# Kernel optimization log

Hardware: AMD Instinct MI355X
Metric: run time of the kernel (lower is better)

Reference implementation:

```python
import jax, jax.numpy as jnp
import numpy as np

D_MODEL = 768
NUM_HEADS = 12
D_K = D_MODEL // NUM_HEADS


def setup_inputs() -> dict:
    key = jax.random.key(0)
    ks = jax.random.split(key, 11)
    B, S = 2, 2048
    sc = 1.0 / np.sqrt(D_MODEL)
    return {
        "q": jax.random.normal(ks[0], (B, S, D_MODEL), jnp.float32),
        "k": jax.random.normal(ks[1], (B, S, D_MODEL), jnp.float32),
        "v": jax.random.normal(ks[2], (B, S, D_MODEL), jnp.float32),
        "w_q": jax.random.normal(ks[3], (D_MODEL, D_MODEL), jnp.float32) * sc,
        "b_q": jnp.zeros((D_MODEL,), jnp.float32),
        "w_k": jax.random.normal(ks[4], (D_MODEL, D_MODEL), jnp.float32) * sc,
        "b_k": jnp.zeros((D_MODEL,), jnp.float32),
        "w_v": jax.random.normal(ks[5], (D_MODEL, D_MODEL), jnp.float32) * sc,
        "b_v": jnp.zeros((D_MODEL,), jnp.float32),
        "w_o": jax.random.normal(ks[6], (D_MODEL, D_MODEL), jnp.float32) * sc,
        "b_o": jnp.zeros((D_MODEL,), jnp.float32),
    }


def _split_heads(x, B):
    # [B, S, D] -> [B, H, S, d_k]
    return x.reshape(B, -1, NUM_HEADS, D_K).transpose(0, 2, 1, 3)


def reference(q, k, v, w_q, b_q, w_k, b_k, w_v, b_v, w_o, b_o):
    B = q.shape[0]
    # torch nn.Linear: y = x @ W.T + b; weights stored [out, in]
    qh = _split_heads(q @ w_q.T + b_q, B)
    kh = _split_heads(k @ w_k.T + b_k, B)
    vh = _split_heads(v @ w_v.T + b_v, B)
    scores = jnp.einsum("bhsd,bhtd->bhst", qh, kh) / jnp.sqrt(jnp.float32(D_K))
    attn = jax.nn.softmax(scores, axis=-1)
    ctx = jnp.einsum("bhst,bhtd->bhsd", attn, vh)
    ctx = ctx.transpose(0, 2, 1, 3).reshape(B, -1, D_MODEL)
    return ctx @ w_o.T + b_o
```

## Files before the change

### kernel.cpp

```cpp
#include <hip/hip_runtime.h>
#include <cstdint>


#define S_LEN 2048
#define NHEAD 12
#define DMODEL 768

typedef short s16x8 __attribute__((ext_vector_type(8)));
typedef float f32x4 __attribute__((ext_vector_type(4)));

#define MFMA16(a, b, c) __builtin_amdgcn_mfma_f32_16x16x32_bf16((a), (b), (c), 0, 0, 0)

__device__ __forceinline__ void lds_dma16(void* lds, const void* g) {
  __builtin_amdgcn_global_load_lds(
      (const __attribute__((address_space(1))) unsigned int*)g,
      (__attribute__((address_space(3))) unsigned int*)lds, 16, 0, 0);
}

__device__ __forceinline__ unsigned int pk_bf16(float a, float b) {
  unsigned int ua = __float_as_uint(a), ub = __float_as_uint(b);
  ua = (ua + 0x7FFFu + ((ua >> 16) & 1u)) >> 16;
  ub = (ub + 0x7FFFu + ((ub >> 16) & 1u)) >> 16;
  return ua | (ub << 16);
}
__device__ __forceinline__ short bf16r(float a) {
  unsigned int ua = __float_as_uint(a);
  return (short)((ua + 0x7FFFu + ((ua >> 16) & 1u)) >> 16);
}
__device__ __forceinline__ unsigned int pk_trunc(float a, float b) {
  return __builtin_amdgcn_perm(__float_as_uint(b), __float_as_uint(a), 0x07060302u);
}
__device__ __forceinline__ float bf16_floor(float a) {
  return __uint_as_float(__float_as_uint(a) & 0xFFFF0000u);
}

__global__ __launch_bounds__(256)
void convert_all(const float* __restrict__ q, const float* __restrict__ k,
                 const float* __restrict__ v,
                 const float* __restrict__ w0, const float* __restrict__ w1,
                 const float* __restrict__ w2, const float* __restrict__ w3,
                 short* __restrict__ qb, short* __restrict__ kb,
                 short* __restrict__ vb,
                 short* __restrict__ o0, short* __restrict__ o1,
                 short* __restrict__ o2, short* __restrict__ o3) {
  int b = blockIdx.x;
  const float* src;
  short* dst;
  if (b < 9216) {
    const int s = b / 3072;
    src = (s == 0) ? q : (s == 1) ? k : v;
    dst = (s == 0) ? qb : (s == 1) ? kb : vb;
    b -= s * 3072;
  } else {
    b -= 9216;
    const int s = b / 576;
    src = (s == 0) ? w0 : (s == 1) ? w1 : (s == 2) ? w2 : w3;
    dst = (s == 0) ? o0 : (s == 1) ? o1 : (s == 2) ? o2 : o3;
    b -= s * 576;
  }
  const long i = ((long)b * 256 + threadIdx.x) * 4;
  float4 f = *(const float4*)(src + i);
  uint2 u;
  u.x = pk_bf16(f.x, f.y);
  u.y = pk_bf16(f.z, f.w);
  *(uint2*)(dst + i) = u;
}

__global__ __launch_bounds__(256)
void qkv_kernel(const short* __restrict__ qb, const short* __restrict__ kb,
                const short* __restrict__ vb,
                const short* __restrict__ wq, const short* __restrict__ wk,
                const short* __restrict__ wv,
                const float* __restrict__ bq, const float* __restrict__ bk,
                const float* __restrict__ bv,
                short* __restrict__ qh, short* __restrict__ kh,
                short* __restrict__ vt) {
  constexpr int K = 768;
  __shared__ short Abuf[128 * 32];
  __shared__ short Bbuf[128 * 32];

  const int L   = blockIdx.x;
  const int xcd = L & 7;
  const int i   = L >> 3;
  const int nt  = i % 6;
  const int pl  = xcd * 12 + i / 6;
  const int z   = pl >> 5;
  const int mt  = pl & 31;
  const int m0  = mt * 128;
  const int n0  = nt * 128;

  const short* A = (z == 0) ? qb : (z == 1) ? kb : vb;
  const short* B = (z == 0) ? wq : (z == 1) ? wk : wv;
  const float* bias = (z == 0) ? bq : (z == 1) ? bk : bv;

  const int tid  = threadIdx.x;
  const int lane = tid & 63;
  const int w    = tid >> 6;
  const int g    = lane >> 4;
  const int c    = lane & 15;
  const int wm   = (w & 1) * 64;
  const int wn   = (w >> 1) * 64;

  const int drow = w * 32 + (lane >> 2);
  const int dcol = (lane & 3) * 8;
  const short* Ag = A + (long)(m0 + drow) * K + dcol;
  const short* Bg = B + (long)(n0 + drow) * K + dcol;
  short* Al0 = &Abuf[w * 1024];
  short* Al1 = &Abuf[w * 1024 + 512];
  short* Bl0 = &Bbuf[w * 1024];
  short* Bl1 = &Bbuf[w * 1024 + 512];

  f32x4 acc[4][4];
#pragma unroll
  for (int a = 0; a < 4; ++a)
#pragma unroll
    for (int b2 = 0; b2 < 4; ++b2) acc[a][b2] = (f32x4){0.f, 0.f, 0.f, 0.f};

  for (int kt = 0; kt < K; kt += 32) {
    lds_dma16(Al0, Ag + kt);
    lds_dma16(Al1, Ag + (long)16 * K + kt);
    lds_dma16(Bl0, Bg + kt);
    lds_dma16(Bl1, Bg + (long)16 * K + kt);
    __syncthreads();

    s16x8 af[4], bf[4];
#pragma unroll
    for (int mb = 0; mb < 4; ++mb)
      af[mb] = *(const s16x8*)&Abuf[(wm + mb * 16 + c) * 32 + g * 8];
#pragma unroll
    for (int nb = 0; nb < 4; ++nb)
      bf[nb] = *(const s16x8*)&Bbuf[(wn + nb * 16 + c) * 32 + g * 8];
#pragma unroll
    for (int mb = 0; mb < 4; ++mb)
#pragma unroll
      for (int nb = 0; nb < 4; ++nb)
        acc[mb][nb] = MFMA16(af[mb], bf[nb], acc[mb][nb]);
    __syncthreads();
  }

  if (z < 2) {
    short* outp = z ? kh : qh;
    const float scale = z ? 1.0f : 0.18033688011112042f;
#pragma unroll
    for (int mb = 0; mb < 4; ++mb) {
#pragma unroll
      for (int nb = 0; nb < 4; ++nb) {
        const int n = n0 + wn + nb * 16 + c;
        const float bvv = bias[n];
        const int hh = n >> 6, d = n & 63;
#pragma unroll
        for (int r = 0; r < 4; ++r) {
          const int m = m0 + wm + mb * 16 + g * 4 + r;
          const int b2 = m >> 11, s = m & 2047;
          const float val = (acc[mb][nb][r] + bvv) * scale;
          outp[(((long)(b2 * NHEAD + hh) * S_LEN + s) << 6) + d] = bf16r(val);
        }
      }
    }
  } else {
#pragma unroll
    for (int mb = 0; mb < 4; ++mb) {
#pragma unroll
      for (int nb = 0; nb < 4; ++nb) {
        const int n = n0 + wn + nb * 16 + c;
        const float bvv = bias[n];
        const int hh = n >> 6, d = n & 63;
        const int m_base = m0 + wm + mb * 16 + g * 4;
        const int b2 = m_base >> 11, t = m_base & 2047;
        uint2 ov;
        ov.x = pk_bf16(acc[mb][nb][0] + bvv, acc[mb][nb][1] + bvv);
        ov.y = pk_bf16(acc[mb][nb][2] + bvv, acc[mb][nb][3] + bvv);
        *(uint2*)(vt + ((long)(b2 * NHEAD + hh) * 64 + d) * S_LEN + t) = ov;
      }
    }
  }
}

__global__ __launch_bounds__(256)
void o_kernel(const short* __restrict__ ctx, const short* __restrict__ wo,
              const float* __restrict__ bo, float* __restrict__ out) {
  constexpr int K = 768;
  __shared__ short Abuf[64 * 32];
  __shared__ short Bbuf[128 * 32];

  const int L   = blockIdx.x;
  const int xcd = L & 7;
  const int i   = L >> 3;
  const int nt  = i % 6;
  const int mt  = xcd * 8 + i / 6;
  const int m0  = mt * 64;
  const int n0  = nt * 128;

  const int tid  = threadIdx.x;
  const int lane = tid & 63;
  const int w    = tid >> 6;
  const int g    = lane >> 4;
  const int c    = lane & 15;
  const int wm   = (w & 1) * 32;
  const int wn   = (w >> 1) * 64;

  const int arow = w * 16 + (lane >> 2);
  const int brow = w * 32 + (lane >> 2);
  const int dcol = (lane & 3) * 8;
  const short* Ag = ctx + (long)(m0 + arow) * K + dcol;
  const short* Bg = wo + (long)(n0 + brow) * K + dcol;
  short* Al = &Abuf[w * 512];
  short* Bl0 = &Bbuf[w * 1024];
  short* Bl1 = &Bbuf[w * 1024 + 512];

  f32x4 acc[2][4];
#pragma unroll
  for (int a = 0; a < 2; ++a)
#pragma unroll
    for (int b2 = 0; b2 < 4; ++b2) acc[a][b2] = (f32x4){0.f, 0.f, 0.f, 0.f};

  for (int kt = 0; kt < K; kt += 32) {
    lds_dma16(Al, Ag + kt);
    lds_dma16(Bl0, Bg + kt);
    lds_dma16(Bl1, Bg + (long)16 * K + kt);
    __syncthreads();

    s16x8 af[2], bf[4];
#pragma unroll
    for (int mb = 0; mb < 2; ++mb)
      af[mb] = *(const s16x8*)&Abuf[(wm + mb * 16 + c) * 32 + g * 8];
#pragma unroll
    for (int nb = 0; nb < 4; ++nb)
      bf[nb] = *(const s16x8*)&Bbuf[(wn + nb * 16 + c) * 32 + g * 8];
#pragma unroll
    for (int mb = 0; mb < 2; ++mb)
#pragma unroll
      for (int nb = 0; nb < 4; ++nb)
        acc[mb][nb] = MFMA16(af[mb], bf[nb], acc[mb][nb]);
    __syncthreads();
  }

#pragma unroll
  for (int mb = 0; mb < 2; ++mb) {
#pragma unroll
    for (int nb = 0; nb < 4; ++nb) {
      const int n = n0 + wn + nb * 16 + c;
      const float bvv = bo[n];
#pragma unroll
      for (int r = 0; r < 4; ++r) {
        const int m = m0 + wm + mb * 16 + g * 4 + r;
        out[(long)m * DMODEL + n] = acc[mb][nb][r] + bvv;
      }
    }
  }
}

__global__ __launch_bounds__(256)
void attn_kernel(const short* __restrict__ Qh, const short* __restrict__ Kh,
                 const short* __restrict__ Vt, short* __restrict__ Ctx) {
  __shared__ short kbuf[2][64 * 64];
  __shared__ short vbuf[2][64 * 64];
  __shared__ short pbuf[4][16 * 64];

  const int tid  = threadIdx.x;
  const int lane = tid & 63;
  const int w    = tid >> 6;
  const int g    = lane >> 4;
  const int c    = lane & 15;
  const int bh   = blockIdx.y;
  const int qs0  = blockIdx.x * 64;
  const long base = (long)bh * S_LEN * 64;
  const short* Qb = Qh + base;
  const short* Kb = Kh + base;
  const short* Vb = Vt + base;

  const long qrow = (long)(qs0 + w * 16 + c) * 64;
  const s16x8 qf0 = *(const s16x8*)(Qb + qrow + g * 8);
  const s16x8 qf1 = *(const s16x8*)(Qb + qrow + 32 + g * 8);

  f32x4 co[4];
#pragma unroll
  for (int i = 0; i < 4; ++i) co[i] = (f32x4){0.f, 0.f, 0.f, 0.f};
  float l_lane = 0.f;

  const int drow  = w * 8 + (lane >> 3);
  const int dchk  = ((lane & 7) ^ (lane >> 3)) * 8;
  const short* kdma = Kb + (long)drow * 64 + dchk;
  const short* vdma = Vb + (long)drow * S_LEN + dchk;

  auto dma_tile = [&](int p, long t0) {
#pragma unroll
    for (int i = 0; i < 2; ++i) {
      lds_dma16(&kbuf[p][(i * 32 + w * 8) * 64], kdma + (t0 + i * 32) * 64);
      lds_dma16(&vbuf[p][(i * 32 + w * 8) * 64], vdma + (long)i * 32 * S_LEN + t0);
    }
  };

  const int cw   = c & 7;
  const int rg0  = ((g)     ^ cw) * 8;
  const int rg1  = ((4 + g) ^ cw) * 8;
  const int pr0 = c * 64 + ((g ^ cw) * 8);
  const int pr1 = c * 64 + (((4 + g) ^ cw) * 8);

  auto step = [&](const short* kb2, const short* vb2) {
    f32x4 st[4];
#pragma unroll
    for (int mb = 0; mb < 4; ++mb) {
      const s16x8 k0 = *(const s16x8*)&kb2[(mb * 16 + c) * 64 + rg0];
      const s16x8 k1 = *(const s16x8*)&kb2[(mb * 16 + c) * 64 + rg1];
      f32x4 z = (f32x4){0.f, 0.f, 0.f, 0.f};
      z = MFMA16(k0, qf0, z);
      z = MFMA16(k1, qf1, z);
      st[mb] = z;
    }
#pragma unroll
    for (int mb = 0; mb < 4; ++mb) {
      float p0 = __builtin_amdgcn_exp2f(st[mb][0]);
      float p1 = __builtin_amdgcn_exp2f(st[mb][1]);
      float p2 = __builtin_amdgcn_exp2f(st[mb][2]);
      float p3 = __builtin_amdgcn_exp2f(st[mb][3]);
      l_lane += bf16_floor(p0) + bf16_floor(p1) + bf16_floor(p2) + bf16_floor(p3);
      uint2 pw;
      pw.x = pk_trunc(p0, p1);
      pw.y = pk_trunc(p2, p3);
      const int pg = ((2 * mb + (g >> 1)) ^ cw) * 8 + (g & 1) * 4;
      *(uint2*)&pbuf[w][c * 64 + pg] = pw;
    }
    const s16x8 pb0 = *(const s16x8*)&pbuf[w][pr0];
    const s16x8 pb1 = *(const s16x8*)&pbuf[w][pr1];
#pragma unroll
    for (int db = 0; db < 4; ++db) {
      const s16x8 v0 = *(const s16x8*)&vb2[(db * 16 + c) * 64 + rg0];
      const s16x8 v1 = *(const s16x8*)&vb2[(db * 16 + c) * 64 + rg1];
      __builtin_amdgcn_s_setprio(1);
      co[db] = MFMA16(v0, pb0, co[db]);
      co[db] = MFMA16(v1, pb1, co[db]);
      __builtin_amdgcn_s_setprio(0);
    }
  };

  constexpr int NT = S_LEN / 64;
  dma_tile(0, 0);
  dma_tile(1, 64);
  int p = 0;
  for (int j = 0; j < NT; ++j) {
    asm volatile("s_waitcnt vmcnt(4)" ::: "memory");
    __builtin_amdgcn_s_barrier();
    __builtin_amdgcn_sched_barrier(0);
    step(kbuf[p], vbuf[p]);
    __builtin_amdgcn_s_barrier();
    const long tn = (j + 2 < NT) ? (long)(j + 2) * 64 : 0;
    dma_tile(p, tn);
    p ^= 1;
  }

  float rs = l_lane;
  rs += __shfl_xor(rs, 16);
  rs += __shfl_xor(rs, 32);
  const float invl = 1.f / rs;

  const int hh = bh % NHEAD;
  const long tok = (long)(bh / NHEAD) * S_LEN + qs0 + w * 16 + c;
#pragma unroll
  for (int db = 0; db < 4; ++db) {
    uint2 ov;
    ov.x = pk_bf16(co[db][0] * invl, co[db][1] * invl);
    ov.y = pk_bf16(co[db][2] * invl, co[db][3] * invl);
    *(uint2*)(Ctx + tok * DMODEL + hh * 64 + db * 16 + g * 4) = ov;
  }
}

extern "C" void kernel_launch(void* const* d_in, const int* in_sizes, int n_in,
                              void* d_out, int out_size, void* d_ws, size_t ws_size,
                              hipStream_t stream) {
  const float* q   = (const float*)d_in[0];
  const float* k   = (const float*)d_in[1];
  const float* v   = (const float*)d_in[2];
  const float* w_q = (const float*)d_in[3];
  const float* b_q = (const float*)d_in[4];
  const float* w_k = (const float*)d_in[5];
  const float* b_k = (const float*)d_in[6];
  const float* w_v = (const float*)d_in[7];
  const float* b_v = (const float*)d_in[8];
  const float* w_o = (const float*)d_in[9];
  const float* b_o = (const float*)d_in[10];
  float* out = (float*)d_out;

  const long NELEM = (long)2 * NHEAD * S_LEN * 64;
  const long WELEM = (long)DMODEL * DMODEL;
  short* qh  = (short*)d_ws;
  short* kh  = qh + NELEM;
  short* vt  = kh + NELEM;
  short* wqb = vt + NELEM;
  short* wkb = wqb + WELEM;
  short* wvb = wkb + WELEM;
  short* wob = wvb + WELEM;
  short* qb  = wob + WELEM;
  short* kb  = qb + NELEM;
  short* vb  = kb + NELEM;
  short* ctx = qb;

  dim3 blk(256);
  convert_all<<<dim3(11520), blk, 0, stream>>>(q, k, v, w_q, w_k, w_v, w_o,
                                               qb, kb, vb, wqb, wkb, wvb, wob);
  qkv_kernel<<<dim3(576), blk, 0, stream>>>(qb, kb, vb, wqb, wkb, wvb,
                                            b_q, b_k, b_v, qh, kh, vt);
  attn_kernel<<<dim3(32, 24), blk, 0, stream>>>(qh, kh, vt, ctx);
  o_kernel<<<dim3(384), blk, 0, stream>>>(ctx, wob, b_o, out);
}
```

Before: 204.7 us.

## Restructure attention kernel onto 32x32 MFMA with register-resident P and split-K waves

Rewrites the attention inner loop to use 32x32x16 bf16 MFMA instead of 16x16x32. The softmax probabilities stay in registers and are rearranged with v_permlane32_swap, which removes the per-wave LDS staging buffer for P. Wave pairs split the key tiles by parity, and their partial outputs and row sums are combined through LDS at the end. K/V loading changes from direct global-to-LDS DMA to register-staged loads that fetch two tiles per phase, and launch bounds request 3 blocks per CU. The risks are extra register pressure, fewer waves covering each query row, and the cost of the final reduction.

```diff
diff --git a/kernel.cpp b/kernel.cpp
--- a/kernel.cpp
+++ b/kernel.cpp
@@ -8,8 +8,10 @@
 
 typedef short s16x8 __attribute__((ext_vector_type(8)));
 typedef float f32x4 __attribute__((ext_vector_type(4)));
+typedef float f32x16 __attribute__((ext_vector_type(16)));
 
 #define MFMA16(a, b, c) __builtin_amdgcn_mfma_f32_16x16x32_bf16((a), (b), (c), 0, 0, 0)
+#define MFMA32(a, b, c) __builtin_amdgcn_mfma_f32_32x32x16_bf16((a), (b), (c), 0, 0, 0)
 
 __device__ __forceinline__ void lds_dma16(void* lds, const void* g) {
   __builtin_amdgcn_global_load_lds(
@@ -250,18 +252,19 @@
   }
 }
 
-__global__ __launch_bounds__(256)
+__global__ __launch_bounds__(256, 3)
 void attn_kernel(const short* __restrict__ Qh, const short* __restrict__ Kh,
                  const short* __restrict__ Vt, short* __restrict__ Ctx) {
   __shared__ short kbuf[2][64 * 64];
   __shared__ short vbuf[2][64 * 64];
-  __shared__ short pbuf[4][16 * 64];
 
   const int tid  = threadIdx.x;
   const int lane = tid & 63;
   const int w    = tid >> 6;
-  const int g    = lane >> 4;
-  const int c    = lane & 15;
+  const int par  = w & 1;
+  const int rh   = w >> 1;
+  const int q32  = lane & 31;
+  const int hi   = lane >> 5;
   const int bh   = blockIdx.y;
   const int qs0  = blockIdx.x * 64;
   const long base = (long)bh * S_LEN * 64;
@@ -269,99 +272,158 @@
   const short* Kb = Kh + base;
   const short* Vb = Vt + base;
 
-  const long qrow = (long)(qs0 + w * 16 + c) * 64;
-  const s16x8 qf0 = *(const s16x8*)(Qb + qrow + g * 8);
-  const s16x8 qf1 = *(const s16x8*)(Qb + qrow + 32 + g * 8);
-
-  f32x4 co[4];
-#pragma unroll
-  for (int i = 0; i < 4; ++i) co[i] = (f32x4){0.f, 0.f, 0.f, 0.f};
+  const long qrow = (long)(qs0 + rh * 32 + q32) * 64;
+  s16x8 qf[4];
+#pragma unroll
+  for (int db = 0; db < 4; ++db)
+    qf[db] = *(const s16x8*)(Qb + qrow + db * 16 + hi * 8);
+
+  f32x16 co0, co1;
+#pragma unroll
+  for (int i = 0; i < 16; ++i) { co0[i] = 0.f; co1[i] = 0.f; }
   float l_lane = 0.f;
 
-  const int drow  = w * 8 + (lane >> 3);
-  const int dchk  = ((lane & 7) ^ (lane >> 3)) * 8;
-  const short* kdma = Kb + (long)drow * 64 + dchk;
-  const short* vdma = Vb + (long)drow * S_LEN + dchk;
-
-  auto dma_tile = [&](int p, long t0) {
-#pragma unroll
-    for (int i = 0; i < 2; ++i) {
-      lds_dma16(&kbuf[p][(i * 32 + w * 8) * 64], kdma + (t0 + i * 32) * 64);
-      lds_dma16(&vbuf[p][(i * 32 + w * 8) * 64], vdma + (long)i * 32 * S_LEN + t0);
-    }
+  const int srow = tid >> 2;
+  const int sq   = tid & 3;
+  const int sw   = srow & 7;
+  const int sg0  = ((2 * sq)     ^ sw) * 8;
+  const int sg1  = ((2 * sq + 1) ^ sw) * 8;
+  const short* kg = Kb + (long)srow * 64 + sq * 16;
+  const short* vg = Vb + (long)srow * S_LEN + sq * 16;
+
+  uint4 rkE0, rkE1, rvE0, rvE1, rkO0, rkO1, rvO0, rvO1;
+  auto fetch_pair = [&](long tE, long tO) {
+    rkE0 = *(const uint4*)(kg + tE * 64);
+    rkE1 = *(const uint4*)(kg + tE * 64 + 8);
+    rvE0 = *(const uint4*)(vg + tE);
+    rvE1 = *(const uint4*)(vg + tE + 8);
+    rkO0 = *(const uint4*)(kg + tO * 64);
+    rkO1 = *(const uint4*)(kg + tO * 64 + 8);
+    rvO0 = *(const uint4*)(vg + tO);
+    rvO1 = *(const uint4*)(vg + tO + 8);
   };
-
-  const int cw   = c & 7;
-  const int rg0  = ((g)     ^ cw) * 8;
-  const int rg1  = ((4 + g) ^ cw) * 8;
-  const int pr0 = c * 64 + ((g ^ cw) * 8);
-  const int pr1 = c * 64 + (((4 + g) ^ cw) * 8);
-
-  auto step = [&](const short* kb2, const short* vb2) {
-    f32x4 st[4];
-#pragma unroll
-    for (int mb = 0; mb < 4; ++mb) {
-      const s16x8 k0 = *(const s16x8*)&kb2[(mb * 16 + c) * 64 + rg0];
-      const s16x8 k1 = *(const s16x8*)&kb2[(mb * 16 + c) * 64 + rg1];
-      f32x4 z = (f32x4){0.f, 0.f, 0.f, 0.f};
-      z = MFMA16(k0, qf0, z);
-      z = MFMA16(k1, qf1, z);
-      st[mb] = z;
-    }
-#pragma unroll
-    for (int mb = 0; mb < 4; ++mb) {
-      float p0 = __builtin_amdgcn_exp2f(st[mb][0]);
-      float p1 = __builtin_amdgcn_exp2f(st[mb][1]);
-      float p2 = __builtin_amdgcn_exp2f(st[mb][2]);
-      float p3 = __builtin_amdgcn_exp2f(st[mb][3]);
-      l_lane += bf16_floor(p0) + bf16_floor(p1) + bf16_floor(p2) + bf16_floor(p3);
-      uint2 pw;
-      pw.x = pk_trunc(p0, p1);
-      pw.y = pk_trunc(p2, p3);
-      const int pg = ((2 * mb + (g >> 1)) ^ cw) * 8 + (g & 1) * 4;
-      *(uint2*)&pbuf[w][c * 64 + pg] = pw;
-    }
-    const s16x8 pb0 = *(const s16x8*)&pbuf[w][pr0];
-    const s16x8 pb1 = *(const s16x8*)&pbuf[w][pr1];
+  auto store_pair = [&]() {
+    *(uint4*)&kbuf[0][srow * 64 + sg0] = rkE0;
+    *(uint4*)&kbuf[0][srow * 64 + sg1] = rkE1;
+    *(uint4*)&vbuf[0][srow * 64 + sg0] = rvE0;
+    *(uint4*)&vbuf[0][srow * 64 + sg1] = rvE1;
+    *(uint4*)&kbuf[1][srow * 64 + sg0] = rkO0;
+    *(uint4*)&kbuf[1][srow * 64 + sg1] = rkO1;
+    *(uint4*)&vbuf[1][srow * 64 + sg0] = rvO0;
+    *(uint4*)&vbuf[1][srow * 64 + sg1] = rvO1;
+  };
+
+  const int tw = lane & 7;
+  int c4[4];
+#pragma unroll
+  for (int i = 0; i < 4; ++i) c4[i] = ((2 * i + hi) ^ tw) * 8;
+  const int row0 = q32 * 64;
+  const int row1 = (32 + q32) * 64;
+  const short* kb2 = kbuf[par];
+  const short* vb2 = vbuf[par];
+
+  auto mkfrag = [&](unsigned a, unsigned b, unsigned c, unsigned d) -> s16x8 {
+    asm("v_permlane32_swap_b32 %0, %1" : "+v"(a), "+v"(c));
+    asm("v_permlane32_swap_b32 %0, %1" : "+v"(b), "+v"(d));
+    uint4 u;
+    u.x = a; u.y = b; u.z = c; u.w = d;
+    return __builtin_bit_cast(s16x8, u);
+  };
+
+  auto step = [&]() {
+    f32x16 s0, s1;
+#pragma unroll
+    for (int i = 0; i < 16; ++i) { s0[i] = 0.f; s1[i] = 0.f; }
+    __builtin_amdgcn_s_setprio(1);
 #pragma unroll
     for (int db = 0; db < 4; ++db) {
-      const s16x8 v0 = *(const s16x8*)&vb2[(db * 16 + c) * 64 + rg0];
-      const s16x8 v1 = *(const s16x8*)&vb2[(db * 16 + c) * 64 + rg1];
-      __builtin_amdgcn_s_setprio(1);
-      co[db] = MFMA16(v0, pb0, co[db]);
-      co[db] = MFMA16(v1, pb1, co[db]);
-      __builtin_amdgcn_s_setprio(0);
-    }
+      const s16x8 k0 = *(const s16x8*)&kb2[row0 + c4[db]];
+      const s16x8 k1 = *(const s16x8*)&kb2[row1 + c4[db]];
+      s0 = MFMA32(k0, qf[db], s0);
+      s1 = MFMA32(k1, qf[db], s1);
+    }
+    __builtin_amdgcn_s_setprio(0);
+    unsigned pk0[8], pk1[8];
+#pragma unroll
+    for (int i = 0; i < 8; ++i) {
+      float a0 = __builtin_amdgcn_exp2f(s0[2 * i]);
+      float b0 = __builtin_amdgcn_exp2f(s0[2 * i + 1]);
+      float a1 = __builtin_amdgcn_exp2f(s1[2 * i]);
+      float b1 = __builtin_amdgcn_exp2f(s1[2 * i + 1]);
+      l_lane += (bf16_floor(a0) + bf16_floor(b0)) +
+                (bf16_floor(a1) + bf16_floor(b1));
+      pk0[i] = pk_trunc(a0, b0);
+      pk1[i] = pk_trunc(a1, b1);
+    }
+    s16x8 pf0 = mkfrag(pk0[0], pk0[1], pk0[2], pk0[3]);
+    s16x8 pf1 = mkfrag(pk0[4], pk0[5], pk0[6], pk0[7]);
+    s16x8 pf2 = mkfrag(pk1[0], pk1[1], pk1[2], pk1[3]);
+    s16x8 pf3 = mkfrag(pk1[4], pk1[5], pk1[6], pk1[7]);
+    __builtin_amdgcn_s_setprio(1);
+#pragma unroll
+    for (int sl = 0; sl < 4; ++sl) {
+      const s16x8 v0 = *(const s16x8*)&vb2[row0 + c4[sl]];
+      const s16x8 v1 = *(const s16x8*)&vb2[row1 + c4[sl]];
+      const s16x8 pf = (sl == 0) ? pf0 : (sl == 1) ? pf1 : (sl == 2) ? pf2 : pf3;
+      co0 = MFMA32(v0, pf, co0);
+      co1 = MFMA32(v1, pf, co1);
+    }
+    __builtin_amdgcn_s_setprio(0);
   };
 
   constexpr int NT = S_LEN / 64;
-  dma_tile(0, 0);
-  dma_tile(1, 64);
-  int p = 0;
-  for (int j = 0; j < NT; ++j) {
-    asm volatile("s_waitcnt vmcnt(4)" ::: "memory");
-    __builtin_amdgcn_s_barrier();
-    __builtin_amdgcn_sched_barrier(0);
-    step(kbuf[p], vbuf[p]);
-    __builtin_amdgcn_s_barrier();
-    const long tn = (j + 2 < NT) ? (long)(j + 2) * 64 : 0;
-    dma_tile(p, tn);
-    p ^= 1;
-  }
-
-  float rs = l_lane;
-  rs += __shfl_xor(rs, 16);
-  rs += __shfl_xor(rs, 32);
-  const float invl = 1.f / rs;
-
-  const int hh = bh % NHEAD;
-  const long tok = (long)(bh / NHEAD) * S_LEN + qs0 + w * 16 + c;
-#pragma unroll
-  for (int db = 0; db < 4; ++db) {
-    uint2 ov;
-    ov.x = pk_bf16(co[db][0] * invl, co[db][1] * invl);
-    ov.y = pk_bf16(co[db][2] * invl, co[db][3] * invl);
-    *(uint2*)(Ctx + tok * DMODEL + hh * 64 + db * 16 + g * 4) = ov;
+  fetch_pair(0, 64);
+  store_pair();
+  for (int ph = 0; ph < NT / 2; ++ph) {
+    __syncthreads();
+    const long tE = (2 * ph + 2 < NT) ? (long)(2 * ph + 2) * 64 : 0;
+    const long tO = (2 * ph + 3 < NT) ? (long)(2 * ph + 3) * 64 : 0;
+    fetch_pair(tE, tO);
+    step();
+    __syncthreads();
+    store_pair();
+  }
+
+  float rs = l_lane + __shfl_xor(l_lane, 32);
+
+  __syncthreads();
+  float* mbuf = (float*)((rh == 0) ? (short*)kbuf : (short*)vbuf);
+  float* mp = mbuf + lane * 36;
+  if (par) {
+#pragma unroll
+    for (int i = 0; i < 4; ++i) {
+      *(float4*)(mp + 4 * i)      = make_float4(co0[4*i], co0[4*i+1], co0[4*i+2], co0[4*i+3]);
+      *(float4*)(mp + 16 + 4 * i) = make_float4(co1[4*i], co1[4*i+1], co1[4*i+2], co1[4*i+3]);
+    }
+    mp[32] = rs;
+  }
+  __syncthreads();
+  if (!par) {
+#pragma unroll
+    for (int i = 0; i < 4; ++i) {
+      float4 a = *(const float4*)(mp + 4 * i);
+      float4 b = *(const float4*)(mp + 16 + 4 * i);
+      co0[4*i] += a.x; co0[4*i+1] += a.y; co0[4*i+2] += a.z; co0[4*i+3] += a.w;
+      co1[4*i] += b.x; co1[4*i+1] += b.y; co1[4*i+2] += b.z; co1[4*i+3] += b.w;
+    }
+    rs += mp[32];
+    const float invl = 1.f / rs;
+
+    const int hh = bh % NHEAD;
+    const long tok = (long)(bh / NHEAD) * S_LEN + qs0 + rh * 32 + q32;
+    short* outp = Ctx + tok * DMODEL + hh * 64;
+#pragma unroll
+    for (int rq = 0; rq < 4; ++rq) {
+      const int d0 = 8 * rq + 4 * hi;
+      uint2 ov;
+      ov.x = pk_bf16(co0[4*rq] * invl, co0[4*rq+1] * invl);
+      ov.y = pk_bf16(co0[4*rq+2] * invl, co0[4*rq+3] * invl);
+      *(uint2*)(outp + d0) = ov;
+      uint2 ov2;
+      ov2.x = pk_bf16(co1[4*rq] * invl, co1[4*rq+1] * invl);
+      ov2.y = pk_bf16(co1[4*rq+2] * invl, co1[4*rq+3] * invl);
+      *(uint2*)(outp + 32 + d0) = ov2;
+    }
   }
 }
 
```

Result: faster. 193.1 us (-5.7%).
